# Kernel optimization log

Measured on AMD Instinct MI355X. Metric: run time of the kernel, lower is better.

The kernel has to match this reference:

```python
import jax, jax.numpy as jnp
import numpy as np

B_, C_, NH_, WS_, HID_ = 8, 512, 16, 7, 2048
HH, WW = 56, 56


def _rel_pos_index(ws):
    coords = np.stack(np.meshgrid(np.arange(ws), np.arange(ws), indexing='ij'))  # (2,ws,ws)
    cf = coords.reshape(2, -1)
    rc = (cf[:, :, None] - cf[:, None, :]).transpose(1, 2, 0)  # (ws2,ws2,2)
    rc[..., 0] += ws - 1
    rc[..., 1] += ws - 1
    rc[..., 0] *= 2 * ws - 1
    return jnp.asarray(rc.sum(-1).reshape(-1))  # (ws2*ws2,)


def _ln(x, g, b, eps):
    mu = x.mean(-1, keepdims=True)
    var = ((x - mu) ** 2).mean(-1, keepdims=True)
    return (x - mu) * jax.lax.rsqrt(var + eps) * g + b


def setup_inputs() -> dict:
    key = jax.random.key(0)
    ks = jax.random.split(key, 8)
    s = lambda k, shape: (jax.random.normal(k, shape, jnp.float32) * 0.02)
    return {
        'x': jax.random.normal(ks[0], (B_, HH * WW, C_), jnp.float32),
        'H': HH, 'W': WW,
        'norm1_g': jnp.ones((C_,), jnp.float32), 'norm1_b': jnp.zeros((C_,), jnp.float32),
        'norm2_g': jnp.ones((C_,), jnp.float32), 'norm2_b': jnp.zeros((C_,), jnp.float32),
        'qkv_w': s(ks[1], (3 * C_, C_)), 'qkv_b': jnp.zeros((3 * C_,), jnp.float32),
        'rpb': s(ks[2], ((2 * WS_ - 1) ** 2, NH_)),
        'fc1_w': s(ks[3], (HID_, C_)), 'fc1_b': jnp.zeros((HID_,), jnp.float32),
        'dw_w': s(ks[4], (HID_, 1, 3, 3)), 'dw_b': jnp.zeros((HID_,), jnp.float32),
        'fc2_w': s(ks[5], (C_, HID_)), 'fc2_b': jnp.zeros((C_,), jnp.float32),
    }


def reference(x, H, W, norm1_g, norm1_b, norm2_g, norm2_b, qkv_w, qkv_b, rpb,
              fc1_w, fc1_b, dw_w, dw_b, fc2_w, fc2_b):
    B, N, C = x.shape
    ws, nh = WS_, NH_
    hd = C // nh
    scale = hd ** -0.5
    ws2 = ws * ws
    nHw, nWw = H // ws, W // ws

    # ---- norm1 + WaveAttention (windowed attention w/ relative position bias) ----
    h = _ln(x, norm1_g, norm1_b, 1e-5)
    qkv = h @ qkv_w.T + qkv_b                                   # [B,N,3C]
    # window partition: [B, nH, ws, nW, ws, 3, nh, hd] -> [3, B*nH*nW, nh, ws2, hd]
    qkv = qkv.reshape(B, nHw, ws, nWw, ws, 3, nh, hd)
    qkv = qkv.transpose(5, 0, 1, 3, 6, 2, 4, 7).reshape(3, B * nHw * nWw, nh, ws2, hd)
    q, k, v = qkv[0], qkv[1], qkv[2]

    attn = jnp.einsum('wnid,wnjd->wnij', q, k) * scale          # [Bw,nh,ws2,ws2]
    bias = rpb[_rel_pos_index(ws)].reshape(ws2, ws2, nh).transpose(2, 0, 1)
    attn = jax.nn.softmax(attn + bias[None], axis=-1)
    out = jnp.einsum('wnij,wnjd->wnid', attn, v)                # [Bw,nh,ws2,hd]
    # window reverse
    out = out.transpose(0, 2, 1, 3).reshape(B, nHw, nWw, ws, ws, C)
    out = out.transpose(0, 1, 3, 2, 4, 5).reshape(B, N, C)
    x = x + out

    # ---- norm2 + PVT2FFN (fc1 -> depthwise 3x3 conv -> GELU -> fc2) ----
    h2 = _ln(x, norm2_g, norm2_b, 1e-5)
    h2 = h2 @ fc1_w.T + fc1_b                                   # [B,N,HID]
    img = h2.reshape(B, H, W, HID_).transpose(0, 3, 1, 2)       # [B,HID,H,W]
    img = jax.lax.conv_general_dilated(img, dw_w, (1, 1), 'SAME',
                                       feature_group_count=HID_)
    img = img + dw_b[None, :, None, None]
    h2 = img.reshape(B, HID_, N).transpose(0, 2, 1)
    h2 = jax.nn.gelu(h2, approximate=False)
    h2 = h2 @ fc2_w.T + fc2_b
    return x + h2
```

## Files before the change

kernel.cpp:

```cpp
#include <hip/hip_runtime.h>
#include <hip/hip_bf16.h>

typedef unsigned short u16;
typedef unsigned int u32;
typedef __attribute__((ext_vector_type(8))) short bf16x8_t;
typedef __attribute__((ext_vector_type(4))) float f32x4_t;
typedef __attribute__((ext_vector_type(8))) u16 u16x8;

constexpr int B_  = 8;
constexpr int C_  = 512;
constexpr int NH_ = 16;
constexpr int HID_= 2048;
constexpr int Hh  = 56, Ww = 56;
constexpr int N_  = Hh * Ww;
constexpr int M_  = B_ * N_;

__device__ __forceinline__ u16 f2bf(float f) {
    u32 u = __float_as_uint(f);
    u32 r = (u + 0x7fffu + ((u >> 16) & 1u)) >> 16;
    return (u16)r;
}
__device__ __forceinline__ float bf2f(u16 v) {
    return __uint_as_float(((u32)v) << 16);
}

__device__ __forceinline__ void gload_lds16(const void* g, void* l) {
    __builtin_amdgcn_global_load_lds(
        (const __attribute__((address_space(1))) u32*)g,
        (__attribute__((address_space(3))) u32*)l, 16, 0, 0);
}

__global__ void cvt_w(const float* __restrict__ qkvw, const float* __restrict__ fc1w,
                      const float* __restrict__ fc2w, u16* __restrict__ oq,
                      u16* __restrict__ o1, u16* __restrict__ o2) {
    int i = blockIdx.x * 256 + threadIdx.x;
    if (i < 3 * C_ * C_) oq[i] = f2bf(qkvw[i]);
    if (i < HID_ * C_) { o1[i] = f2bf(fc1w[i]); o2[i] = f2bf(fc2w[i]); }
}

__global__ __launch_bounds__(256) void ln_kernel(const float* __restrict__ x,
        const float* __restrict__ g, const float* __restrict__ b, u16* __restrict__ out) {
    int lane = threadIdx.x & 63, wv = threadIdx.x >> 6;
    size_t row = (size_t)blockIdx.x * 4 + wv;
    const float4* xr = (const float4*)(x + row * C_);
    float4 a = xr[lane * 2], c = xr[lane * 2 + 1];
    float s  = a.x + a.y + a.z + a.w + c.x + c.y + c.z + c.w;
    float ss = a.x*a.x + a.y*a.y + a.z*a.z + a.w*a.w + c.x*c.x + c.y*c.y + c.z*c.z + c.w*c.w;
    #pragma unroll
    for (int off = 1; off < 64; off <<= 1) {
        s  += __shfl_xor(s, off);
        ss += __shfl_xor(ss, off);
    }
    float mean = s * (1.0f / C_);
    float var  = ss * (1.0f / C_) - mean * mean;
    float rstd = rsqrtf(var + 1e-5f);
    const float4* g4 = (const float4*)g;
    const float4* b4 = (const float4*)b;
    float4 g0 = g4[lane*2], g1 = g4[lane*2+1], b0 = b4[lane*2], b1 = b4[lane*2+1];
    u16x8 o;
    o[0] = f2bf((a.x - mean) * rstd * g0.x + b0.x);
    o[1] = f2bf((a.y - mean) * rstd * g0.y + b0.y);
    o[2] = f2bf((a.z - mean) * rstd * g0.z + b0.z);
    o[3] = f2bf((a.w - mean) * rstd * g0.w + b0.w);
    o[4] = f2bf((c.x - mean) * rstd * g1.x + b1.x);
    o[5] = f2bf((c.y - mean) * rstd * g1.y + b1.y);
    o[6] = f2bf((c.z - mean) * rstd * g1.z + b1.z);
    o[7] = f2bf((c.w - mean) * rstd * g1.w + b1.w);
    *(u16x8*)&out[row * C_ + lane * 8] = o;
}

template<bool RES, bool OUT_BF16>
__global__ __launch_bounds__(256) void gemm_bt(
        const u16* __restrict__ A, const u16* __restrict__ B,
        const float* __restrict__ bias, const float* __restrict__ res,
        void* __restrict__ Cout, int M, int N, int K) {
    __shared__ __align__(16) u16 As[2][128 * 32];
    __shared__ __align__(16) u16 Bs[2][128 * 32];
    const int tid = threadIdx.x;
    const int lane = tid & 63;
    const int wv = tid >> 6;
    const int bm = blockIdx.x, bn = blockIdx.y;

    const int r0 = lane >> 2;
    const int gcb = ((lane & 3) ^ ((lane >> 3) & 3));

    const u16* aBase = A + (size_t)(bm * 128) * K;
    const u16* bBase = B + (size_t)(bn * 128) * K;

    f32x4_t acc[4][4];
    f32x4_t zero = {0.f, 0.f, 0.f, 0.f};
    #pragma unroll
    for (int i = 0; i < 4; i++)
        #pragma unroll
        for (int j = 0; j < 4; j++) acc[i][j] = zero;

    const int mo = (wv >> 1) * 64, no = (wv & 1) * 64;
    const int fr = lane & 15;
    const int g4 = lane >> 4;
    const int kkey = (fr >> 1) & 3;
    const int pos = (g4 ^ kkey) * 8;

    auto stage = [&](int buf, int k0) {
        const int ko = k0 + gcb * 8;
        gload_lds16(aBase + (size_t)(wv * 16 + r0) * K + ko,       &As[buf][(wv * 16) * 32]);
        gload_lds16(aBase + (size_t)((wv + 4) * 16 + r0) * K + ko, &As[buf][((wv + 4) * 16) * 32]);
        gload_lds16(bBase + (size_t)(wv * 16 + r0) * K + ko,       &Bs[buf][(wv * 16) * 32]);
        gload_lds16(bBase + (size_t)((wv + 4) * 16 + r0) * K + ko, &Bs[buf][((wv + 4) * 16) * 32]);
    };

    stage(0, 0);
    __syncthreads();
    int buf = 0;
    for (int k0 = 0; k0 < K; k0 += 32, buf ^= 1) {
        if (k0 + 32 < K) stage(buf ^ 1, k0 + 32);
        bf16x8_t af[4], bfr[4];
        #pragma unroll
        for (int mt = 0; mt < 4; mt++)
            af[mt] = *(const bf16x8_t*)&As[buf][(mo + mt * 16 + fr) * 32 + pos];
        #pragma unroll
        for (int nt = 0; nt < 4; nt++)
            bfr[nt] = *(const bf16x8_t*)&Bs[buf][(no + nt * 16 + fr) * 32 + pos];
        #pragma unroll
        for (int mt = 0; mt < 4; mt++)
            #pragma unroll
            for (int nt = 0; nt < 4; nt++)
                acc[mt][nt] = __builtin_amdgcn_mfma_f32_16x16x32_bf16(af[mt], bfr[nt], acc[mt][nt], 0, 0, 0);
        __syncthreads();
    }

    #pragma unroll
    for (int mt = 0; mt < 4; mt++) {
        #pragma unroll
        for (int r = 0; r < 4; r++) {
            int row = bm * 128 + mo + mt * 16 + (lane >> 4) * 4 + r;
            #pragma unroll
            for (int nt = 0; nt < 4; nt++) {
                int col = bn * 128 + no + nt * 16 + (lane & 15);
                float v = acc[mt][nt][r] + bias[col];
                if constexpr (RES) v += res[(size_t)row * N + col];
                if constexpr (OUT_BF16) ((u16*)Cout)[(size_t)row * N + col] = f2bf(v);
                else ((float*)Cout)[(size_t)row * N + col] = v;
            }
        }
    }
}

constexpr int QS = 40;
constexpr int VS = 72;
constexpr int PS = 72;

__global__ __launch_bounds__(256) void attn_kernel(
        const u16* __restrict__ qkv, const float* __restrict__ rpb,
        u16* __restrict__ aout) {
    __shared__ __align__(16) u16 q_s[64 * QS];
    __shared__ __align__(16) u16 k_s[64 * QS];
    __shared__ __align__(16) u16 vT_s[32 * VS];
    __shared__ __align__(16) u16 p_s[64 * PS];
    const int tid = threadIdx.x, lane = tid & 63, wv = tid >> 6;
    const int wh = blockIdx.x;
    const int head = wh & 15, w = wh >> 4;
    const int b = w >> 6, win = w & 63, bh = win >> 3, bw = win & 7;

    {
        int i = tid >> 2, dc = (tid & 3) * 8;
        if (i < 49) {
            int n = (bh * 7 + i / 7) * Ww + (bw * 7 + i % 7);
            const u16* base = qkv + ((size_t)(b * N_ + n)) * (3 * C_) + head * 32 + dc;
            *(u16x8*)&q_s[i * QS + dc] = *(const u16x8*)(base);
            *(u16x8*)&k_s[i * QS + dc] = *(const u16x8*)(base + C_);
        } else {
            u16x8 z = {0,0,0,0,0,0,0,0};
            *(u16x8*)&q_s[i * QS + dc] = z;
            *(u16x8*)&k_s[i * QS + dc] = z;
        }
    }
    for (int f = tid; f < 64 * 32; f += 256) {
        int i = f >> 5, d = f & 31;
        u16 val = 0;
        if (i < 49) {
            int n = (bh * 7 + i / 7) * Ww + (bw * 7 + i % 7);
            val = qkv[((size_t)(b * N_ + n)) * (3 * C_) + 2 * C_ + head * 32 + d];
        }
        vT_s[d * VS + i] = val;
    }
    __syncthreads();

    f32x4_t zero = {0.f, 0.f, 0.f, 0.f};
    f32x4_t s[4];
    bf16x8_t aq = *(const bf16x8_t*)&q_s[(wv * 16 + (lane & 15)) * QS + (lane >> 4) * 8];
    #pragma unroll
    for (int nt = 0; nt < 4; nt++) {
        bf16x8_t bk = *(const bf16x8_t*)&k_s[(nt * 16 + (lane & 15)) * QS + (lane >> 4) * 8];
        s[nt] = __builtin_amdgcn_mfma_f32_16x16x32_bf16(aq, bk, zero, 0, 0, 0);
    }

    const float scale = 0.17677669529663687f;
    #pragma unroll
    for (int r = 0; r < 4; r++) {
        int row = wv * 16 + (lane >> 4) * 4 + r;
        int qy = row / 7, qx = row - qy * 7;
        float pv[4];
        float m = -1e30f;
        #pragma unroll
        for (int nt = 0; nt < 4; nt++) {
            int col = nt * 16 + (lane & 15);
            float bias;
            if (row < 49 && col < 49) {
                int ky = col / 7, kx = col - ky * 7;
                bias = rpb[((qy - ky + 6) * 13 + (qx - kx + 6)) * NH_ + head];
            } else bias = -1e30f;
            float v = s[nt][r] * scale + bias;
            pv[nt] = v;
            m = fmaxf(m, v);
        }
        #pragma unroll
        for (int off = 1; off < 16; off <<= 1) m = fmaxf(m, __shfl_xor(m, off));
        float sum = 0.f;
        #pragma unroll
        for (int nt = 0; nt < 4; nt++) { pv[nt] = __expf(pv[nt] - m); sum += pv[nt]; }
        #pragma unroll
        for (int off = 1; off < 16; off <<= 1) sum += __shfl_xor(sum, off);
        float inv = 1.0f / sum;
        #pragma unroll
        for (int nt = 0; nt < 4; nt++)
            p_s[row * PS + nt * 16 + (lane & 15)] = f2bf(pv[nt] * inv);
    }
    __syncthreads();

    f32x4_t o[2] = {zero, zero};
    #pragma unroll
    for (int kt = 0; kt < 2; kt++) {
        bf16x8_t ap = *(const bf16x8_t*)&p_s[(wv * 16 + (lane & 15)) * PS + kt * 32 + (lane >> 4) * 8];
        #pragma unroll
        for (int nt = 0; nt < 2; nt++) {
            bf16x8_t bv = *(const bf16x8_t*)&vT_s[(nt * 16 + (lane & 15)) * VS + kt * 32 + (lane >> 4) * 8];
            o[nt] = __builtin_amdgcn_mfma_f32_16x16x32_bf16(ap, bv, o[nt], 0, 0, 0);
        }
    }
    u16* obase = aout + ((size_t)(w * 16 + head)) * 49 * 32;
    #pragma unroll
    for (int nt = 0; nt < 2; nt++) {
        #pragma unroll
        for (int r = 0; r < 4; r++) {
            int row = wv * 16 + (lane >> 4) * 4 + r;
            if (row < 49)
                obase[row * 32 + nt * 16 + (lane & 15)] = f2bf(o[nt][r]);
        }
    }
}

__global__ __launch_bounds__(256) void wrev_ln(const float* __restrict__ x,
        const u16* __restrict__ aout, const float* __restrict__ g,
        const float* __restrict__ bt, float* __restrict__ x2, u16* __restrict__ h) {
    int lane = threadIdx.x & 63, wvv = threadIdx.x >> 6;
    int m = blockIdx.x * 4 + wvv;
    int b = m / N_, n = m - b * N_;
    int iy = n / Ww, ix = n - iy * Ww;
    int w = b * 64 + (iy / 7) * 8 + (ix / 7);
    int pos = (iy % 7) * 7 + (ix % 7);
    int head = lane >> 2, d0 = (lane & 3) * 8;
    u16x8 ao = *(const u16x8*)&aout[(((size_t)w * 16 + head) * 49 + pos) * 32 + d0];
    const float4* xr = (const float4*)(x + (size_t)m * C_ + lane * 8);
    float4 a = xr[0], c = xr[1];
    float v[8];
    v[0] = a.x + bf2f(ao[0]); v[1] = a.y + bf2f(ao[1]);
    v[2] = a.z + bf2f(ao[2]); v[3] = a.w + bf2f(ao[3]);
    v[4] = c.x + bf2f(ao[4]); v[5] = c.y + bf2f(ao[5]);
    v[6] = c.z + bf2f(ao[6]); v[7] = c.w + bf2f(ao[7]);
    float s = 0.f, ss = 0.f;
    #pragma unroll
    for (int j = 0; j < 8; j++) { s += v[j]; ss += v[j] * v[j]; }
    #pragma unroll
    for (int off = 1; off < 64; off <<= 1) {
        s  += __shfl_xor(s, off);
        ss += __shfl_xor(ss, off);
    }
    float mean = s * (1.0f / C_);
    float var  = ss * (1.0f / C_) - mean * mean;
    float rstd = rsqrtf(var + 1e-5f);
    float4 o0 = {v[0], v[1], v[2], v[3]}, o1 = {v[4], v[5], v[6], v[7]};
    float4* x2r = (float4*)(x2 + (size_t)m * C_ + lane * 8);
    x2r[0] = o0; x2r[1] = o1;
    const float4* g4 = (const float4*)(g + lane * 8);
    const float4* b4 = (const float4*)(bt + lane * 8);
    float4 g0 = g4[0], g1 = g4[1], bb0 = b4[0], bb1 = b4[1];
    u16x8 o;
    o[0] = f2bf((v[0] - mean) * rstd * g0.x + bb0.x);
    o[1] = f2bf((v[1] - mean) * rstd * g0.y + bb0.y);
    o[2] = f2bf((v[2] - mean) * rstd * g0.z + bb0.z);
    o[3] = f2bf((v[3] - mean) * rstd * g0.w + bb0.w);
    o[4] = f2bf((v[4] - mean) * rstd * g1.x + bb1.x);
    o[5] = f2bf((v[5] - mean) * rstd * g1.y + bb1.y);
    o[6] = f2bf((v[6] - mean) * rstd * g1.z + bb1.z);
    o[7] = f2bf((v[7] - mean) * rstd * g1.w + bb1.w);
    *(u16x8*)&h[(size_t)m * C_ + lane * 8] = o;
}

__global__ __launch_bounds__(256) void dwconv_gelu(const u16* __restrict__ in,
        const float* __restrict__ w, const float* __restrict__ bias, u16* __restrict__ out) {
    const int t = threadIdx.x;
    const int blk = blockIdx.x;
    const int half = blk & 1;
    const int byp = blk >> 1;
    const int yp = byp % 28;
    const int b = byp / 28;
    const int y0 = yp * 2;
    const int c0 = t * 8;

    float wr[9][8];
    #pragma unroll
    for (int k = 0; k < 9; k++)
        #pragma unroll
        for (int j = 0; j < 8; j++) wr[k][j] = w[(c0 + j) * 9 + k];
    float bs[8];
    #pragma unroll
    for (int j = 0; j < 8; j++) bs[j] = bias[c0 + j];

    u16x8 zerov = {0,0,0,0,0,0,0,0};
    auto ldcol = [&](int xx, u16x8* col) {
        #pragma unroll
        for (int dy = 0; dy < 4; dy++) {
            int yy = y0 + dy - 1;
            bool ok = (yy >= 0 && yy < Hh && xx >= 0 && xx < Ww);
            col[dy] = ok ? *(const u16x8*)&in[(((size_t)b * Hh + yy) * Ww + xx) * HID_ + c0] : zerov;
        }
    };

    int xs = half * 28;
    u16x8 wA[4], wB[4], wC[4];
    ldcol(xs - 1, wA);
    ldcol(xs, wB);
    for (int x = xs; x < xs + 28; x++) {
        ldcol(x + 1, wC);
        float acc0[8], acc1[8];
        #pragma unroll
        for (int j = 0; j < 8; j++) { acc0[j] = bs[j]; acc1[j] = bs[j]; }
        #pragma unroll
        for (int dy = 0; dy < 3; dy++)
            #pragma unroll
            for (int j = 0; j < 8; j++) {
                acc0[j] += bf2f(wA[dy][j]) * wr[dy * 3 + 0][j];
                acc0[j] += bf2f(wB[dy][j]) * wr[dy * 3 + 1][j];
                acc0[j] += bf2f(wC[dy][j]) * wr[dy * 3 + 2][j];
                acc1[j] += bf2f(wA[dy + 1][j]) * wr[dy * 3 + 0][j];
                acc1[j] += bf2f(wB[dy + 1][j]) * wr[dy * 3 + 1][j];
                acc1[j] += bf2f(wC[dy + 1][j]) * wr[dy * 3 + 2][j];
            }
        u16x8 o0, o1;
        #pragma unroll
        for (int j = 0; j < 8; j++) {
            float v0 = acc0[j];
            o0[j] = f2bf(0.5f * v0 * (1.0f + erff(v0 * 0.70710678118654752f)));
            float v1 = acc1[j];
            o1[j] = f2bf(0.5f * v1 * (1.0f + erff(v1 * 0.70710678118654752f)));
        }
        *(u16x8*)&out[(((size_t)b * Hh + y0) * Ww + x) * HID_ + c0] = o0;
        *(u16x8*)&out[(((size_t)b * Hh + y0 + 1) * Ww + x) * HID_ + c0] = o1;
        #pragma unroll
        for (int dy = 0; dy < 4; dy++) { wA[dy] = wB[dy]; wB[dy] = wC[dy]; }
    }
}

extern "C" void kernel_launch(void* const* d_in, const int* in_sizes, int n_in,
                              void* d_out, int out_size, void* d_ws, size_t ws_size,
                              hipStream_t stream) {
    const float* x    = (const float*)d_in[0];
    const float* n1g  = (const float*)d_in[3];
    const float* n1b  = (const float*)d_in[4];
    const float* n2g  = (const float*)d_in[5];
    const float* n2b  = (const float*)d_in[6];
    const float* qkvw = (const float*)d_in[7];
    const float* qkvb = (const float*)d_in[8];
    const float* rpb  = (const float*)d_in[9];
    const float* fc1w = (const float*)d_in[10];
    const float* fc1b = (const float*)d_in[11];
    const float* dww  = (const float*)d_in[12];
    const float* dwb  = (const float*)d_in[13];
    const float* fc2w = (const float*)d_in[14];
    const float* fc2b = (const float*)d_in[15];

    char* ws = (char*)d_ws;
    float* x2  = (float*)(ws);
    u16*   h   = (u16*)(ws + 51380224);
    u16*   qkvo= (u16*)(ws + 77070336);
    u16*   aout= (u16*)(ws + 154140672);
    u16*   f1o = (u16*)(ws + 154140672);
    u16*   cvo = (u16*)(ws + 51380224);
    u16*   wq  = (u16*)(ws + 256901120);
    u16*   w1  = (u16*)(ws + 256901120 + 1572864);
    u16*   w2  = (u16*)(ws + 256901120 + 1572864 + 2097152);

    cvt_w<<<dim3(4096), dim3(256), 0, stream>>>(qkvw, fc1w, fc2w, wq, w1, w2);
    ln_kernel<<<dim3(M_ / 4), dim3(256), 0, stream>>>(x, n1g, n1b, h);
    gemm_bt<false, true><<<dim3(M_ / 128, 1536 / 128), dim3(256), 0, stream>>>(
        h, wq, qkvb, nullptr, (void*)qkvo, M_, 1536, 512);
    attn_kernel<<<dim3(B_ * 64 * NH_), dim3(256), 0, stream>>>(qkvo, rpb, aout);
    wrev_ln<<<dim3(M_ / 4), dim3(256), 0, stream>>>(x, aout, n2g, n2b, x2, h);
    gemm_bt<false, true><<<dim3(M_ / 128, 2048 / 128), dim3(256), 0, stream>>>(
        h, w1, fc1b, nullptr, (void*)f1o, M_, 2048, 512);
    dwconv_gelu<<<dim3(B_ * 28 * 2), dim3(256), 0, stream>>>(f1o, dww, dwb, cvo);
    gemm_bt<true, false><<<dim3(M_ / 128, 512 / 128), dim3(256), 0, stream>>>(
        cvo, w2, fc2b, x2, d_out, M_, 512, 2048);
}
```

Measured before the change: 575.6 us.

## Remap GEMM blocks for XCD-local A reuse, use K=64 steps, split dwconv finer

The GEMM launch becomes a 1D grid. Each block is remapped so that groups of four N-tiles sharing the same M-tile land on the same XCD, which lets them share A tiles in that XCD's L2. The K loop now loads 64-wide slabs with one sync before compute, replacing the double-buffered 32-wide prefetch. That halves the number of barriers but no longer overlaps loads with MFMA. The depthwise conv is split into quarter rows to launch more blocks, at the cost of more halo reloads.

```diff
diff --git a/kernel.cpp b/kernel.cpp
--- a/kernel.cpp
+++ b/kernel.cpp
@@ -73,13 +73,22 @@
 __global__ __launch_bounds__(256) void gemm_bt(
         const u16* __restrict__ A, const u16* __restrict__ B,
         const float* __restrict__ bias, const float* __restrict__ res,
-        void* __restrict__ Cout, int M, int N, int K) {
-    __shared__ __align__(16) u16 As[2][128 * 32];
-    __shared__ __align__(16) u16 Bs[2][128 * 32];
+        void* __restrict__ Cout, int M, int N, int K,
+        int nbm, int nbn, int nGroups) {
+    const int id = blockIdx.x;
+    const int xcd = id & 7, slot = id >> 3;
+    const int j = slot & 3;
+    const int gidx = xcd + 8 * (slot >> 2);
+    if (gidx >= nGroups) return;
+    const int bm = gidx % nbm;
+    const int bn = (gidx / nbm) * 4 + j;
+    if (bn >= nbn) return;
+
+    __shared__ __align__(16) u16 As[2 * 128 * 32];
+    __shared__ __align__(16) u16 Bs[2 * 128 * 32];
     const int tid = threadIdx.x;
     const int lane = tid & 63;
     const int wv = tid >> 6;
-    const int bm = blockIdx.x, bn = blockIdx.y;
 
     const int r0 = lane >> 2;
     const int gcb = ((lane & 3) ^ ((lane >> 3) & 3));
@@ -92,7 +101,7 @@
     #pragma unroll
     for (int i = 0; i < 4; i++)
         #pragma unroll
-        for (int j = 0; j < 4; j++) acc[i][j] = zero;
+        for (int jj = 0; jj < 4; jj++) acc[i][jj] = zero;
 
     const int mo = (wv >> 1) * 64, no = (wv & 1) * 64;
     const int fr = lane & 15;
@@ -100,31 +109,32 @@
     const int kkey = (fr >> 1) & 3;
     const int pos = (g4 ^ kkey) * 8;
 
-    auto stage = [&](int buf, int k0) {
-        const int ko = k0 + gcb * 8;
-        gload_lds16(aBase + (size_t)(wv * 16 + r0) * K + ko,       &As[buf][(wv * 16) * 32]);
-        gload_lds16(aBase + (size_t)((wv + 4) * 16 + r0) * K + ko, &As[buf][((wv + 4) * 16) * 32]);
-        gload_lds16(bBase + (size_t)(wv * 16 + r0) * K + ko,       &Bs[buf][(wv * 16) * 32]);
-        gload_lds16(bBase + (size_t)((wv + 4) * 16 + r0) * K + ko, &Bs[buf][((wv + 4) * 16) * 32]);
-    };
-
-    stage(0, 0);
-    __syncthreads();
-    int buf = 0;
-    for (int k0 = 0; k0 < K; k0 += 32, buf ^= 1) {
-        if (k0 + 32 < K) stage(buf ^ 1, k0 + 32);
-        bf16x8_t af[4], bfr[4];
-        #pragma unroll
-        for (int mt = 0; mt < 4; mt++)
-            af[mt] = *(const bf16x8_t*)&As[buf][(mo + mt * 16 + fr) * 32 + pos];
-        #pragma unroll
-        for (int nt = 0; nt < 4; nt++)
-            bfr[nt] = *(const bf16x8_t*)&Bs[buf][(no + nt * 16 + fr) * 32 + pos];
-        #pragma unroll
-        for (int mt = 0; mt < 4; mt++)
+    for (int k0 = 0; k0 < K; k0 += 64) {
+        #pragma unroll
+        for (int p = 0; p < 2; p++) {
+            const int ko = k0 + p * 32 + gcb * 8;
+            gload_lds16(aBase + (size_t)(wv * 16 + r0) * K + ko,       &As[p * 4096 + (wv * 16) * 32]);
+            gload_lds16(aBase + (size_t)((wv + 4) * 16 + r0) * K + ko, &As[p * 4096 + ((wv + 4) * 16) * 32]);
+            gload_lds16(bBase + (size_t)(wv * 16 + r0) * K + ko,       &Bs[p * 4096 + (wv * 16) * 32]);
+            gload_lds16(bBase + (size_t)((wv + 4) * 16 + r0) * K + ko, &Bs[p * 4096 + ((wv + 4) * 16) * 32]);
+        }
+        __syncthreads();
+
+        #pragma unroll
+        for (int ks = 0; ks < 2; ks++) {
+            bf16x8_t af[4], bfr[4];
+            #pragma unroll
+            for (int mt = 0; mt < 4; mt++)
+                af[mt] = *(const bf16x8_t*)&As[ks * 4096 + (mo + mt * 16 + fr) * 32 + pos];
             #pragma unroll
             for (int nt = 0; nt < 4; nt++)
-                acc[mt][nt] = __builtin_amdgcn_mfma_f32_16x16x32_bf16(af[mt], bfr[nt], acc[mt][nt], 0, 0, 0);
+                bfr[nt] = *(const bf16x8_t*)&Bs[ks * 4096 + (no + nt * 16 + fr) * 32 + pos];
+            #pragma unroll
+            for (int mt = 0; mt < 4; mt++)
+                #pragma unroll
+                for (int nt = 0; nt < 4; nt++)
+                    acc[mt][nt] = __builtin_amdgcn_mfma_f32_16x16x32_bf16(af[mt], bfr[nt], acc[mt][nt], 0, 0, 0);
+        }
         __syncthreads();
     }
 
@@ -269,7 +279,7 @@
     v[6] = c.z + bf2f(ao[6]); v[7] = c.w + bf2f(ao[7]);
     float s = 0.f, ss = 0.f;
     #pragma unroll
-    for (int j = 0; j < 8; j++) { s += v[j]; ss += v[j] * v[j]; }
+    for (int jj = 0; jj < 8; jj++) { s += v[jj]; ss += v[jj] * v[jj]; }
     #pragma unroll
     for (int off = 1; off < 64; off <<= 1) {
         s  += __shfl_xor(s, off);
@@ -300,8 +310,8 @@
         const float* __restrict__ w, const float* __restrict__ bias, u16* __restrict__ out) {
     const int t = threadIdx.x;
     const int blk = blockIdx.x;
-    const int half = blk & 1;
-    const int byp = blk >> 1;
+    const int xq = blk & 3;
+    const int byp = blk >> 2;
     const int yp = byp % 28;
     const int b = byp / 28;
     const int y0 = yp * 2;
@@ -326,11 +336,11 @@
         }
     };
 
-    int xs = half * 28;
+    int xs = xq * 14;
     u16x8 wA[4], wB[4], wC[4];
     ldcol(xs - 1, wA);
     ldcol(xs, wB);
-    for (int x = xs; x < xs + 28; x++) {
+    for (int x = xs; x < xs + 14; x++) {
         ldcol(x + 1, wC);
         float acc0[8], acc1[8];
         #pragma unroll
@@ -390,15 +400,17 @@
     u16*   w1  = (u16*)(ws + 256901120 + 1572864);
     u16*   w2  = (u16*)(ws + 256901120 + 1572864 + 2097152);
 
+    auto ggrid = [](int nGroups) { return 32 * ((nGroups + 7) / 8); };
+
     cvt_w<<<dim3(4096), dim3(256), 0, stream>>>(qkvw, fc1w, fc2w, wq, w1, w2);
     ln_kernel<<<dim3(M_ / 4), dim3(256), 0, stream>>>(x, n1g, n1b, h);
-    gemm_bt<false, true><<<dim3(M_ / 128, 1536 / 128), dim3(256), 0, stream>>>(
-        h, wq, qkvb, nullptr, (void*)qkvo, M_, 1536, 512);
+    gemm_bt<false, true><<<dim3(ggrid(588)), dim3(256), 0, stream>>>(
+        h, wq, qkvb, nullptr, (void*)qkvo, M_, 1536, 512, 196, 12, 588);
     attn_kernel<<<dim3(B_ * 64 * NH_), dim3(256), 0, stream>>>(qkvo, rpb, aout);
     wrev_ln<<<dim3(M_ / 4), dim3(256), 0, stream>>>(x, aout, n2g, n2b, x2, h);
-    gemm_bt<false, true><<<dim3(M_ / 128, 2048 / 128), dim3(256), 0, stream>>>(
-        h, w1, fc1b, nullptr, (void*)f1o, M_, 2048, 512);
-    dwconv_gelu<<<dim3(B_ * 28 * 2), dim3(256), 0, stream>>>(f1o, dww, dwb, cvo);
-    gemm_bt<true, false><<<dim3(M_ / 128, 512 / 128), dim3(256), 0, stream>>>(
-        cvo, w2, fc2b, x2, d_out, M_, 512, 2048);
-}
+    gemm_bt<false, true><<<dim3(ggrid(784)), dim3(256), 0, stream>>>(
+        h, w1, fc1b, nullptr, (void*)f1o, M_, 2048, 512, 196, 16, 784);
+    dwconv_gelu<<<dim3(B_ * 28 * 4), dim3(256), 0, stream>>>(f1o, dww, dwb, cvo);
+    gemm_bt<true, false><<<dim3(ggrid(196)), dim3(256), 0, stream>>>(
+        cvo, w2, fc2b, x2, d_out, M_, 512, 2048, 196, 4, 196);
+}
```

Result: faster. 541.5 us (-5.9%).
